# Performance work log

Hardware: AMD Instinct MI355X
Metric: run time of the kernel (lower is better)

## Reference

```python
import jax, jax.numpy as jnp
import numpy as np

PS = 32
EMBED_DIM = 768
IN_CH = 3
IMG = 1024
NUM_PATCHES = 992  # ini_row = i for H=1024, so need i+32 <= 1024
SPIKE_IDX = np.array([5, 300, 800])
SPIKE_VAL = 1.0e6  # makes val ~= 23.94 < 24 -> nearest size 16 -> subdivided


def _token_layout(iw_np, num_patches, ps, H):
    """Replicates the module's data-dependent patch-size / subpatch-position logic.
    Returns static (rows, cols, sizes) for every output token, in emission order."""
    avg = iw_np.mean()
    val = np.minimum(ps * avg ** 0.05 / iw_np ** 0.05, float(ps))
    choices = np.array([32, 16, 8, 4], dtype=np.float64)  # argmin picks first on tie, like min(list)
    sizes = choices[np.argmin(np.abs(val[:, None] - choices[None, :]), axis=1)].astype(np.int64)
    rows, cols, szs = [], [], []
    for i in range(num_patches):
        ini_col = (i * ps) % H
        ini_row = (i * ps * ps) // H
        s = int(sizes[i])
        if 3 < s < ps:
            ns = ps // s  # num_subpatches; subpatch_size == s
            for j in range(ns):
                rows.append(ini_row + (j * s) // ns)
                cols.append(ini_col + (j * s) % (ns * s))
                szs.append(s)
        else:
            rows.append(ini_row)
            cols.append(ini_col)
            szs.append(ps)
    return np.asarray(rows), np.asarray(cols), np.asarray(szs)


def _embed(x, W, b, rows, cols, szs, ps):
    E, C = W.shape[0], W.shape[1]
    B = x.shape[0]
    T = szs.shape[0]
    out = jnp.zeros((B, T, E), dtype=x.dtype)
    for s in np.unique(szs):
        s = int(s)
        idx = np.nonzero(szs == s)[0]  # static token slots for this size group
        r, c = rows[idx], cols[idx]
        if s == ps:
            Wf = W
        else:
            kd = ps // s  # fold the ps x ps kernel down to s x s, as in the module
            Wf = W.reshape(E, C, kd, kd, s, s).sum(axis=(2, 3))
        ar = np.arange(s)
        # gather [B, C, K, s, s] sub-patches with static advanced indexing
        patches = x[:, :, r[:, None, None] + ar[None, :, None], c[:, None, None] + ar[None, None, :]]
        tok = jnp.einsum('bckhw,echw->bke', patches, Wf) + b  # stride==kernel -> 1 token each
        out = out.at[:, jnp.asarray(idx), :].set(tok)
    return out


def setup_inputs() -> dict:
    key = jax.random.key(0)
    k_x, k_w, k_iw, k_b = jax.random.split(key, 4)
    x = jax.random.normal(k_x, (8, IN_CH, IMG, IMG), dtype=jnp.float32)
    iw = jax.random.uniform(k_iw, (1, NUM_PATCHES), dtype=jnp.float32, minval=0.5, maxval=1.5)
    iw = iw.at[0, SPIKE_IDX].set(SPIKE_VAL)  # 3 high-importance patches -> size-16 subdivision
    W = jax.random.normal(k_w, (EMBED_DIM, IN_CH, PS, PS), dtype=jnp.float32) * 0.02
    b = jax.random.normal(k_b, (EMBED_DIM,), dtype=jnp.float32) * 0.02
    return {"x": x, "importance_weights": iw, "W": W, "b": b, "num_patches": NUM_PATCHES}


def reference(x, importance_weights, W, b, num_patches):
    iw = np.asarray(importance_weights)[0]
    rows, cols, szs = _token_layout(iw, int(num_patches), PS, x.shape[3])
    return _embed(x, W, b, rows, cols, szs, PS)  # [B, T, E]
```

## Files before the change

kernel.cpp:

```cpp
#include <hip/hip_runtime.h>


typedef __attribute__((ext_vector_type(8))) short bf16x8;
typedef __attribute__((ext_vector_type(4))) float f32x4;

#define K_DIM 3072
#define N_DIM 768

__device__ __forceinline__ unsigned short f2bf(float f) {
  unsigned int u = __float_as_uint(f);
  u += 0x7fffu + ((u >> 16) & 1u);
  return (unsigned short)(u >> 16);
}

__device__ __forceinline__ void gload16(const void* g, void* l) {
  __builtin_amdgcn_global_load_lds(
      (const __attribute__((address_space(1))) void*)g,
      (__attribute__((address_space(3))) void*)l, 16, 0, 0);
}

__global__ __launch_bounds__(1024)
void prep_kernel(const float* __restrict__ W, unsigned short* __restrict__ Wb, int w4,
                 const float* __restrict__ iw, int P,
                 int* __restrict__ tokBase, int* __restrict__ tokMask, int NB_W) {
  int bid = blockIdx.x;
  int tid = threadIdx.x;
  if (bid < NB_W) {
    int idx = bid * 1024 + tid;
    if (idx < w4) {
      float4 f = *(const float4*)(W + (size_t)idx * 4);
      ushort4 o;
      o.x = f2bf(f.x); o.y = f2bf(f.y); o.z = f2bf(f.z); o.w = f2bf(f.w);
      *(ushort4*)(Wb + (size_t)idx * 4) = o;
    }
    return;
  }
  __shared__ double s_wsum[16];
  __shared__ double s_avg;
  __shared__ int s_cnt[1024];
  float v = (tid < P) ? iw[tid] : 0.0f;
  double d = (double)v;
#pragma unroll
  for (int off = 32; off > 0; off >>= 1) d += __shfl_down(d, off, 64);
  if ((tid & 63) == 0) s_wsum[tid >> 6] = d;
  __syncthreads();
  if (tid == 0) {
    double s = 0.0;
    for (int i = 0; i < 16; ++i) s += s_wsum[i];
    s_avg = s / (double)P;
  }
  __syncthreads();
  int cnt = 0, sz = 32;
  if (tid < P) {
    double val = 32.0 * pow(s_avg / (double)v, 0.05);
    if (val > 32.0) val = 32.0;
    sz = (val >= 24.0) ? 32 : (val >= 12.0) ? 16 : (val >= 6.0) ? 8 : 4;
    cnt = (sz < 32) ? (32 / sz) : 1;
  }
  s_cnt[tid] = cnt;
  __syncthreads();
  for (int dl = 1; dl < 1024; dl <<= 1) {
    int add = (tid >= dl) ? s_cnt[tid - dl] : 0;
    __syncthreads();
    s_cnt[tid] += add;
    __syncthreads();
  }
  if (tid < P) {
    int off = s_cnt[tid] - cnt;
    int ini_col = (tid * 32) & 1023;
    int ini_row = (tid * 32 * 32) >> 10;
    if (sz == 32) {
      tokBase[off] = ini_row * 1024 + ini_col;
      tokMask[off] = 31;
    } else {
      int ns = 32 / sz;
      for (int j = 0; j < ns; ++j) {
        int r = ini_row + (j * sz) / ns;
        int c = ini_col + ((j * sz) & 31);
        tokBase[off + j] = r * 1024 + c;
        tokMask[off + j] = sz - 1;
      }
    }
  }
}

__global__ __launch_bounds__(256)
void gather_kernel(const float* __restrict__ x,
                   const int* __restrict__ tokBase,
                   const int* __restrict__ tokMask,
                   unsigned short* __restrict__ Ab) {
  int t = blockIdx.x;
  int b = blockIdx.y;
  int T = gridDim.x;
  int m = b * T + t;
  int base = tokBase[t];
  int mask = tokMask[t];
  int sh = __popc(mask);
  const float* xb = x + (size_t)b * 3145728 + (size_t)base;
  unsigned short* arow = Ab + (size_t)m * K_DIM;
#pragma unroll
  for (int it = 0; it < 3; ++it) {
    int g = it * 256 + threadIdx.x;
    int p = g * 4;
    int c = p >> 10;
    int f = p & 1023;
    int h = (f >> sh) & mask;
    int w = f & mask;
    float4 fv = *(const float4*)(xb + (size_t)c * 1048576 + h * 1024 + w);
    ushort4 o;
    o.x = f2bf(fv.x); o.y = f2bf(fv.y); o.z = f2bf(fv.z); o.w = f2bf(fv.w);
    *(ushort4*)(arow + p) = o;
  }
}

__global__ __launch_bounds__(256, 3)
void gemm_kernel(const unsigned short* __restrict__ A, const unsigned short* __restrict__ Wb,
                 const float* __restrict__ bias, float* __restrict__ out, int Mtot) {
  __shared__ unsigned short lds[2][12288];
  int tid = threadIdx.x;
  int lane = tid & 63;
  int wave = tid >> 6;
  int wr = wave >> 1, wc = wave & 1;

  int lin = blockIdx.x;
  int nwg = gridDim.x;
  int q8 = nwg >> 3, r8 = nwg & 7;
  int xcd = lin & 7, slot = lin >> 3;
  int wg = (xcd < r8) ? xcd * (q8 + 1) + slot
                      : r8 * (q8 + 1) + (xcd - r8) * q8 + slot;
  int mBase = (wg / 12) * 128;
  int nBase = (wg % 12) * 64;

  f32x4 acc[4][2] = {};

  int lrow = lane >> 3;
  int schunk = (lane & 7) ^ lrow;
  const unsigned short* Ag = A + (size_t)(mBase + wave * 32 + lrow) * K_DIM + schunk * 8;
  const unsigned short* Bg = Wb + (size_t)(nBase + wave * 16 + lrow) * K_DIM + schunk * 8;
  unsigned short* Adst0 = &lds[0][(wave * 32) * 64] + lane * 8;
  unsigned short* Bdst0 = &lds[0][8192 + (wave * 16) * 64] + lane * 8;

#define STAGE(BUF, KOFF)                                                    \
  {                                                                         \
    _Pragma("unroll")                                                       \
    for (int inst = 0; inst < 4; ++inst)                                    \
      gload16(Ag + (size_t)(inst * 8) * K_DIM + (KOFF),                     \
              Adst0 + (size_t)(BUF) * 12288 + inst * 512);                  \
    _Pragma("unroll")                                                       \
    for (int inst = 0; inst < 2; ++inst)                                    \
      gload16(Bg + (size_t)(inst * 8) * K_DIM + (KOFF),                     \
              Bdst0 + (size_t)(BUF) * 12288 + inst * 512);                  \
  }

  int rr = lane & 15, q = lane >> 4;
  int r7 = rr & 7;

#define COMPUTE(BUF)                                                        \
  {                                                                         \
    const unsigned short* A_ = &lds[BUF][0];                                \
    const unsigned short* B_ = &lds[BUF][8192];                             \
    _Pragma("unroll")                                                       \
    for (int kh = 0; kh < 2; ++kh) {                                        \
      bf16x8 aF[4], bF[2];                                                  \
      _Pragma("unroll")                                                     \
      for (int i = 0; i < 4; ++i)                                           \
        aF[i] = *(const bf16x8*)&A_[(wr * 64 + i * 16 + rr) * 64 +          \
                                    ((kh * 4 + q) ^ r7) * 8];               \
      _Pragma("unroll")                                                     \
      for (int j = 0; j < 2; ++j)                                           \
        bF[j] = *(const bf16x8*)&B_[(wc * 32 + j * 16 + rr) * 64 +          \
                                    ((kh * 4 + q) ^ r7) * 8];               \
      _Pragma("unroll")                                                     \
      for (int i = 0; i < 4; ++i)                                           \
        _Pragma("unroll")                                                   \
        for (int j = 0; j < 2; ++j)                                         \
          acc[i][j] = __builtin_amdgcn_mfma_f32_16x16x32_bf16(aF[i], bF[j], \
                                                              acc[i][j], 0, 0, 0); \
    }                                                                       \
  }

  STAGE(0, 0)
  __syncthreads();
  int buf = 0;
  for (int k0 = 0; k0 < K_DIM; k0 += 64) {
    if (k0 + 64 < K_DIM) {
      if (buf == 0) STAGE(1, k0 + 64) else STAGE(0, k0 + 64)
    }
    if (buf == 0) COMPUTE(0) else COMPUTE(1)
    __syncthreads();
    buf ^= 1;
  }
#undef STAGE
#undef COMPUTE

#pragma unroll
  for (int j = 0; j < 2; ++j) {
    int n = nBase + wc * 32 + j * 16 + rr;
    float bv = bias[n];
#pragma unroll
    for (int i = 0; i < 4; ++i) {
      int mrow = mBase + wr * 64 + i * 16 + q * 4;
#pragma unroll
      for (int r2 = 0; r2 < 4; ++r2) {
        int m = mrow + r2;
        if (m < Mtot) out[(size_t)m * N_DIM + n] = acc[i][j][r2] + bv;
      }
    }
  }
}

extern "C" void kernel_launch(void* const* d_in, const int* in_sizes, int n_in,
                              void* d_out, int out_size, void* d_ws, size_t ws_size,
                              hipStream_t stream) {
  const float* x  = (const float*)d_in[0];
  const float* iw = (const float*)d_in[1];
  const float* W  = (const float*)d_in[2];
  const float* b  = (const float*)d_in[3];
  int P = in_sizes[1];
  int B = in_sizes[0] / (3 * 1024 * 1024);
  int E = in_sizes[3];
  int T = out_size / (B * E);
  int Mtot = B * T;
  int Mpad = (Mtot + 127) & ~127;

  char* ws = (char*)d_ws;
  int* tokBase = (int*)ws;
  int* tokMask = (int*)(ws + 32768);
  unsigned short* Wb = (unsigned short*)(ws + 65536);
  unsigned short* Ab = (unsigned short*)(ws + 65536 + (size_t)E * K_DIM * 2);

  int w4 = E * K_DIM / 4;
  int NB_W = (w4 + 1023) / 1024;
  prep_kernel<<<NB_W + 1, 1024, 0, stream>>>(W, Wb, w4, iw, P, tokBase, tokMask, NB_W);

  dim3 gGrid(T, B);
  gather_kernel<<<gGrid, 256, 0, stream>>>(x, tokBase, tokMask, Ab);


  dim3 grid((N_DIM / 64) * (Mpad / 128));
  gemm_kernel<<<grid, 256, 0, stream>>>(Ab, Wb, b, (float*)d_out, Mtot);
}
```

Before: 240.2 us.

## Enlarge GEMM tile to 192x128 with 8 waves and triple-buffered LDS pipeline

The GEMM moves from 128x64 tiles with 4 waves and double buffering to 192x128 tiles with 8 waves and a three-stage LDS ring. Global-to-LDS loads are split into A and B halves interleaved across the two k-halves, with explicit vmcnt waits, raw barriers and setprio around the MFMA blocks. The goal is more data reuse per tile and better overlap of loads with MFMA work. In exchange it uses more LDS (about 120 KB), launches fewer workgroups (Mtot≈8000 gives about 42x6 tiles), and the hardcoded iteration count assumes K=3072. Since the gather pads nothing, A rows past Mtot in the last M tile may be read past the valid data.

```diff
diff --git a/kernel.cpp b/kernel.cpp
--- a/kernel.cpp
+++ b/kernel.cpp
@@ -6,6 +6,8 @@
 
 #define K_DIM 3072
 #define N_DIM 768
+#define BM 192
+#define BN 128
 
 __device__ __forceinline__ unsigned short f2bf(float f) {
   unsigned int u = __float_as_uint(f);
@@ -113,14 +115,14 @@
   }
 }
 
-__global__ __launch_bounds__(256, 3)
+__global__ __launch_bounds__(512)
 void gemm_kernel(const unsigned short* __restrict__ A, const unsigned short* __restrict__ Wb,
                  const float* __restrict__ bias, float* __restrict__ out, int Mtot) {
-  __shared__ unsigned short lds[2][12288];
+  __shared__ unsigned short lds[3][20480];
   int tid = threadIdx.x;
   int lane = tid & 63;
   int wave = tid >> 6;
-  int wr = wave >> 1, wc = wave & 1;
+  int wrM = wave >> 1, wrN = wave & 1;
 
   int lin = blockIdx.x;
   int nwg = gridDim.x;
@@ -128,78 +130,100 @@
   int xcd = lin & 7, slot = lin >> 3;
   int wg = (xcd < r8) ? xcd * (q8 + 1) + slot
                       : r8 * (q8 + 1) + (xcd - r8) * q8 + slot;
-  int mBase = (wg / 12) * 128;
-  int nBase = (wg % 12) * 64;
-
-  f32x4 acc[4][2] = {};
+  int mBase = (wg / 6) * BM;
+  int nBase = (wg % 6) * BN;
+
+  f32x4 acc[3][4] = {};
 
   int lrow = lane >> 3;
   int schunk = (lane & 7) ^ lrow;
-  const unsigned short* Ag = A + (size_t)(mBase + wave * 32 + lrow) * K_DIM + schunk * 8;
+  const unsigned short* Ag = A + (size_t)(mBase + wave * 24 + lrow) * K_DIM + schunk * 8;
   const unsigned short* Bg = Wb + (size_t)(nBase + wave * 16 + lrow) * K_DIM + schunk * 8;
-  unsigned short* Adst0 = &lds[0][(wave * 32) * 64] + lane * 8;
-  unsigned short* Bdst0 = &lds[0][8192 + (wave * 16) * 64] + lane * 8;
-
-#define STAGE(BUF, KOFF)                                                    \
-  {                                                                         \
-    _Pragma("unroll")                                                       \
-    for (int inst = 0; inst < 4; ++inst)                                    \
+  unsigned short* Adst0 = &lds[0][(wave * 24) * 64] + lane * 8;
+  unsigned short* Bdst0 = &lds[0][12288 + (wave * 16) * 64] + lane * 8;
+
+#define STAGE_A(BUF, KOFF)                                                  \
+    _Pragma("unroll")                                                       \
+    for (int inst = 0; inst < 3; ++inst)                                    \
       gload16(Ag + (size_t)(inst * 8) * K_DIM + (KOFF),                     \
-              Adst0 + (size_t)(BUF) * 12288 + inst * 512);                  \
+              Adst0 + (size_t)(BUF) * 20480 + inst * 512);
+
+#define STAGE_B(BUF, KOFF)                                                  \
     _Pragma("unroll")                                                       \
     for (int inst = 0; inst < 2; ++inst)                                    \
       gload16(Bg + (size_t)(inst * 8) * K_DIM + (KOFF),                     \
-              Bdst0 + (size_t)(BUF) * 12288 + inst * 512);                  \
-  }
+              Bdst0 + (size_t)(BUF) * 20480 + inst * 512);
 
   int rr = lane & 15, q = lane >> 4;
   int r7 = rr & 7;
 
-#define COMPUTE(BUF)                                                        \
+#define PH(BUF, KH, STG, WAITC)                                             \
   {                                                                         \
-    const unsigned short* A_ = &lds[BUF][0];                                \
-    const unsigned short* B_ = &lds[BUF][8192];                             \
-    _Pragma("unroll")                                                       \
-    for (int kh = 0; kh < 2; ++kh) {                                        \
-      bf16x8 aF[4], bF[2];                                                  \
+    bf16x8 aF[3], bF[4];                                                    \
+    _Pragma("unroll")                                                       \
+    for (int i = 0; i < 3; ++i)                                             \
+      aF[i] = *(const bf16x8*)&lds[BUF][(wrM * 48 + i * 16 + rr) * 64 +     \
+                                        (((KH) * 4 + q) ^ r7) * 8];         \
+    _Pragma("unroll")                                                       \
+    for (int j = 0; j < 4; ++j)                                             \
+      bF[j] = *(const bf16x8*)&lds[BUF][12288 +                             \
+                                        (wrN * 64 + j * 16 + rr) * 64 +     \
+                                        (((KH) * 4 + q) ^ r7) * 8];         \
+    STG                                                                     \
+    WAITC                                                                   \
+    __builtin_amdgcn_s_barrier();                                           \
+    asm volatile("s_waitcnt lgkmcnt(0)" ::: "memory");                      \
+    __builtin_amdgcn_sched_barrier(0);                                      \
+    __builtin_amdgcn_s_setprio(1);                                          \
+    _Pragma("unroll")                                                       \
+    for (int i = 0; i < 3; ++i)                                             \
       _Pragma("unroll")                                                     \
-      for (int i = 0; i < 4; ++i)                                           \
-        aF[i] = *(const bf16x8*)&A_[(wr * 64 + i * 16 + rr) * 64 +          \
-                                    ((kh * 4 + q) ^ r7) * 8];               \
-      _Pragma("unroll")                                                     \
-      for (int j = 0; j < 2; ++j)                                           \
-        bF[j] = *(const bf16x8*)&B_[(wc * 32 + j * 16 + rr) * 64 +          \
-                                    ((kh * 4 + q) ^ r7) * 8];               \
-      _Pragma("unroll")                                                     \
-      for (int i = 0; i < 4; ++i)                                           \
-        _Pragma("unroll")                                                   \
-        for (int j = 0; j < 2; ++j)                                         \
-          acc[i][j] = __builtin_amdgcn_mfma_f32_16x16x32_bf16(aF[i], bF[j], \
-                                                              acc[i][j], 0, 0, 0); \
-    }                                                                       \
-  }
-
-  STAGE(0, 0)
-  __syncthreads();
-  int buf = 0;
-  for (int k0 = 0; k0 < K_DIM; k0 += 64) {
-    if (k0 + 64 < K_DIM) {
-      if (buf == 0) STAGE(1, k0 + 64) else STAGE(0, k0 + 64)
-    }
-    if (buf == 0) COMPUTE(0) else COMPUTE(1)
-    __syncthreads();
-    buf ^= 1;
-  }
-#undef STAGE
-#undef COMPUTE
-
-#pragma unroll
-  for (int j = 0; j < 2; ++j) {
-    int n = nBase + wc * 32 + j * 16 + rr;
+      for (int j = 0; j < 4; ++j)                                           \
+        acc[i][j] = __builtin_amdgcn_mfma_f32_16x16x32_bf16(aF[i], bF[j],   \
+                                                            acc[i][j], 0, 0, 0); \
+    __builtin_amdgcn_s_setprio(0);                                          \
+    __builtin_amdgcn_s_barrier();                                           \
+  }
+
+#define VM5 asm volatile("s_waitcnt vmcnt(5)" ::: "memory");
+#define VM0 asm volatile("s_waitcnt vmcnt(0)" ::: "memory");
+#define NOP
+
+#define ITER(BUF, SBUF, KOFF)                                               \
+  PH(BUF, 0, STAGE_A(SBUF, KOFF), NOP)                                      \
+  PH(BUF, 1, STAGE_B(SBUF, KOFF), VM5)
+
+  STAGE_A(0, 0) STAGE_B(0, 0)
+  STAGE_A(1, 64) STAGE_B(1, 64)
+  VM5
+  __builtin_amdgcn_s_barrier();
+
+  for (int g = 0; g < 15; ++g) {
+    int k = g * 192;
+    ITER(0, 2, k + 128)
+    ITER(1, 0, k + 192)
+    ITER(2, 1, k + 256)
+  }
+  ITER(0, 2, 3008)
+  PH(1, 0, NOP, NOP)
+  PH(1, 1, NOP, VM0)
+  PH(2, 0, NOP, NOP)
+  PH(2, 1, NOP, NOP)
+#undef ITER
+#undef PH
+#undef STAGE_A
+#undef STAGE_B
+#undef VM5
+#undef VM0
+#undef NOP
+
+#pragma unroll
+  for (int j = 0; j < 4; ++j) {
+    int n = nBase + wrN * 64 + j * 16 + rr;
     float bv = bias[n];
 #pragma unroll
-    for (int i = 0; i < 4; ++i) {
-      int mrow = mBase + wr * 64 + i * 16 + q * 4;
+    for (int i = 0; i < 3; ++i) {
+      int mrow = mBase + wrM * 48 + i * 16 + q * 4;
 #pragma unroll
       for (int r2 = 0; r2 < 4; ++r2) {
         int m = mrow + r2;
@@ -221,7 +245,7 @@
   int E = in_sizes[3];
   int T = out_size / (B * E);
   int Mtot = B * T;
-  int Mpad = (Mtot + 127) & ~127;
+  int mTiles = (Mtot + BM - 1) / BM;
 
   char* ws = (char*)d_ws;
   int* tokBase = (int*)ws;
@@ -237,6 +261,6 @@
   gather_kernel<<<gGrid, 256, 0, stream>>>(x, tokBase, tokMask, Ab);
 
 
-  dim3 grid((N_DIM / 64) * (Mpad / 128));
-  gemm_kernel<<<grid, 256, 0, stream>>>(Ab, Wb, b, (float*)d_out, Mtot);
-}
+  dim3 grid((N_DIM / BN) * mTiles);
+  gemm_kernel<<<grid, 512, 0, stream>>>(Ab, Wb, b, (float*)d_out, Mtot);
+}
```

After: 224.8 us. 6.4% less time.
